# Kernel tuning notes

Measured on AMD Instinct MI355X. Metric: run time of the kernel, lower is better.

## Reference

```python
import jax, jax.numpy as jnp
import numpy as np

B, S, D, H = 4, 2048, 768, 12
HD = D // H
SCALE = HD ** -0.5


def setup_inputs() -> dict:
    key = jax.random.key(0)
    ks = jax.random.split(key, 9)
    std = D ** -0.5
    x = jax.random.normal(ks[0], (B, S, D), dtype=jnp.float32)
    Wq = jax.random.normal(ks[1], (D, D), dtype=jnp.float32) * std
    Wk = jax.random.normal(ks[2], (D, D), dtype=jnp.float32) * std
    Wv = jax.random.normal(ks[3], (D, D), dtype=jnp.float32) * std
    Wo = jax.random.normal(ks[4], (D, D), dtype=jnp.float32) * std
    bq = jax.random.normal(ks[5], (D,), dtype=jnp.float32) * 0.01
    bk = jax.random.normal(ks[6], (D,), dtype=jnp.float32) * 0.01
    bv = jax.random.normal(ks[7], (D,), dtype=jnp.float32) * 0.01
    bo = jax.random.normal(ks[8], (D,), dtype=jnp.float32) * 0.01
    return {"x": x, "Wq": Wq, "bq": bq, "Wk": Wk, "bk": bk,
            "Wv": Wv, "bv": bv, "Wo": Wo, "bo": bo}


def reference(x, Wq, bq, Wk, bk, Wv, bv, Wo, bo):
    b, s, _ = x.shape
    # projections (torch Linear: y = x @ W.T + b)
    q = (x @ Wq.T + bq).reshape(b, s, H, HD).transpose(0, 2, 1, 3)  # [B,H,S,HD]
    k = (x @ Wk.T + bk).reshape(b, s, H, HD).transpose(0, 2, 1, 3)
    v = (x @ Wv.T + bv).reshape(b, s, H, HD).transpose(0, 2, 1, 3)
    attn = jnp.einsum('bhqd,bhkd->bhqk', q, k) * SCALE
    attn = jax.nn.softmax(attn, axis=-1)  # dropout is identity in eval mode
    out = jnp.einsum('bhqk,bhkd->bhqd', attn, v)
    out = out.transpose(0, 2, 1, 3).reshape(b, s, D)
    return out @ Wo.T + bo
```

## Files before the change

kernel.cpp:

```cpp
#include <hip/hip_runtime.h>

#define LOG2E 1.4426950408889634f
#define QSCALE (0.125f * LOG2E)

typedef __attribute__((ext_vector_type(8))) __bf16 bf8_t;
typedef __attribute__((ext_vector_type(4))) float f4_t;

__device__ __forceinline__ unsigned short f2bf(float f) {
  unsigned int u = __float_as_uint(f);
  u += 0x7fff + ((u >> 16) & 1);
  return (unsigned short)(u >> 16);
}

__device__ __forceinline__ void async16(const void* g, void* l) {
  __builtin_amdgcn_global_load_lds(
      (const __attribute__((address_space(1))) void*)g,
      (__attribute__((address_space(3))) void*)l, 16, 0, 0);
}

__device__ __forceinline__ int swm(int r) {
  return ((r & 3) << 4) | ((r & 8) << 3);
}
__device__ __forceinline__ int swzoff(int row, int cb) {
  return (row << 7) + (cb ^ swm(row));
}

__global__ void cvt_multi(const float* __restrict__ x,
                          const float* __restrict__ w0, const float* __restrict__ w1,
                          const float* __restrict__ w2, const float* __restrict__ w3,
                          unsigned short* __restrict__ xb,
                          unsigned short* __restrict__ d0, unsigned short* __restrict__ d1,
                          unsigned short* __restrict__ d2, unsigned short* __restrict__ d3) {
  const int NX = 1572864;
  const int NW = 147456;
  const int total = NX + 4 * NW;
  int i = blockIdx.x * blockDim.x + threadIdx.x;
  int stride = gridDim.x * blockDim.x;
  for (; i < total; i += stride) {
    const float* s;
    unsigned short* d;
    int off;
    if (i < NX) {
      s = x; d = xb; off = i;
    } else {
      int j = i - NX;
      int wsel = j / NW;
      off = j - wsel * NW;
      s = (wsel == 0) ? w0 : (wsel == 1) ? w1 : (wsel == 2) ? w2 : w3;
      d = (wsel == 0) ? d0 : (wsel == 1) ? d1 : (wsel == 2) ? d2 : d3;
    }
    float4 v = ((const float4*)s)[off];
    ushort4 o;
    o.x = f2bf(v.x); o.y = f2bf(v.y); o.z = f2bf(v.z); o.w = f2bf(v.w);
    ((ushort4*)d)[off] = o;
  }
}

__device__ __forceinline__ void gemm_core(const unsigned short* __restrict__ A,
                                          const unsigned short* __restrict__ Bm,
                                          int i0, int j0,
                                          char* lsA, char* lsB,
                                          f4_t (&acc)[4][4]) {
  const int tid = threadIdx.x;
  const int l = tid & 63;
  const int wi = (tid >> 6) >> 1, wj = (tid >> 6) & 1;
  for (int k0 = 0; k0 < 768; k0 += 64) {
#pragma unroll
    for (int u = 0; u < 4; ++u) {
      int p = (u * 256 + tid) * 16;
      int r = p >> 7, cb = p & 127;
      int c = cb ^ swm(r);
      async16((const char*)A + ((size_t)(i0 + r) * 768 + k0) * 2 + c, lsA + p);
      async16((const char*)Bm + ((size_t)(j0 + r) * 768 + k0) * 2 + c, lsB + p);
    }
    __syncthreads();
#pragma unroll
    for (int ks = 0; ks < 2; ++ks) {
      bf8_t af[4], bfr[4];
#pragma unroll
      for (int mi = 0; mi < 4; ++mi)
        af[mi] = *(const bf8_t*)(lsA + swzoff(wi * 64 + mi * 16 + (l & 15),
                                              ks * 64 + ((l >> 4) << 4)));
#pragma unroll
      for (int nj = 0; nj < 4; ++nj)
        bfr[nj] = *(const bf8_t*)(lsB + swzoff(wj * 64 + nj * 16 + (l & 15),
                                               ks * 64 + ((l >> 4) << 4)));
      __builtin_amdgcn_s_setprio(1);
#pragma unroll
      for (int mi = 0; mi < 4; ++mi)
#pragma unroll
        for (int nj = 0; nj < 4; ++nj)
          acc[mi][nj] = __builtin_amdgcn_mfma_f32_16x16x32_bf16(
              af[mi], bfr[nj], acc[mi][nj], 0, 0, 0);
      __builtin_amdgcn_s_setprio(0);
    }
    __syncthreads();
  }
}

__global__ __launch_bounds__(256) void proj_qkv(
    const unsigned short* __restrict__ xb,
    const unsigned short* __restrict__ wq,
    const unsigned short* __restrict__ wk,
    const unsigned short* __restrict__ wv,
    const float* __restrict__ bq, const float* __restrict__ bk,
    const float* __restrict__ bv,
    unsigned short* __restrict__ qo, unsigned short* __restrict__ ko,
    unsigned short* __restrict__ vto) {
  __shared__ char lsA[16384], lsB[16384];
  const int bx = (blockIdx.x & 7) * 144 + (blockIdx.x >> 3);
  const int z = bx / 384, r = bx % 384;
  int it, jt;
  const unsigned short *A, *Bm;
  const float* bias;
  if (z == 0)      { A = wq; Bm = xb; bias = bq; it = r % 6;  jt = r / 6;  }
  else if (z == 1) { A = wk; Bm = xb; bias = bk; it = r % 6;  jt = r / 6;  }
  else             { A = xb; Bm = wv; bias = bv; it = r % 64; jt = r / 64; }
  const int i0 = it * 128, j0 = jt * 128;
  f4_t acc[4][4] = {};
  gemm_core(A, Bm, i0, j0, lsA, lsB, acc);

  const int tid = threadIdx.x, l = tid & 63;
  const int wi = (tid >> 6) >> 1, wj = (tid >> 6) & 1;
#pragma unroll
  for (int mi = 0; mi < 4; ++mi) {
#pragma unroll
    for (int nj = 0; nj < 4; ++nj) {
      int ib = i0 + wi * 64 + mi * 16 + ((l >> 4) << 2);
      int j  = j0 + wj * 64 + nj * 16 + (l & 15);
      f4_t v = acc[mi][nj];
      if (z < 2) {
        float4 bs = *(const float4*)(bias + ib);
        float sc = (z == 0) ? QSCALE : 1.0f;
        ushort4 o;
        o.x = f2bf((v[0] + bs.x) * sc);
        o.y = f2bf((v[1] + bs.y) * sc);
        o.z = f2bf((v[2] + bs.z) * sc);
        o.w = f2bf((v[3] + bs.w) * sc);
        int bb = j >> 11, s = j & 2047;
        int h = ib >> 6, d = ib & 63;
        unsigned short* dst = (z == 0) ? qo : ko;
        *(ushort4*)(dst + (((size_t)(bb * 12 + h) * 2048 + s) << 6) + d) = o;
      } else {
        float bvs = bias[j];
        ushort4 o;
        o.x = f2bf(v[0] + bvs); o.y = f2bf(v[1] + bvs);
        o.z = f2bf(v[2] + bvs); o.w = f2bf(v[3] + bvs);
        int bb = ib >> 11, s4 = ib & 2047;
        int h = j >> 6, d = j & 63;
        *(ushort4*)(vto + ((size_t)((bb * 12 + h) * 64 + d)) * 2048 + s4) = o;
      }
    }
  }
}

__global__ __launch_bounds__(256) void proj_o(
    const unsigned short* __restrict__ attnb, const unsigned short* __restrict__ wo,
    const float* __restrict__ bo, float* __restrict__ outp) {
  __shared__ char lsA[16384], lsB[16384];
  const int bx = (blockIdx.x & 7) * 48 + (blockIdx.x >> 3);
  const int it = bx % 6, jt = bx / 6;
  const int i0 = it * 128, j0 = jt * 128;
  f4_t acc[4][4] = {};
  gemm_core(wo, attnb, i0, j0, lsA, lsB, acc);
  const int tid = threadIdx.x, l = tid & 63;
  const int wi = (tid >> 6) >> 1, wj = (tid >> 6) & 1;
#pragma unroll
  for (int mi = 0; mi < 4; ++mi) {
#pragma unroll
    for (int nj = 0; nj < 4; ++nj) {
      int ib = i0 + wi * 64 + mi * 16 + ((l >> 4) << 2);
      int j  = j0 + wj * 64 + nj * 16 + (l & 15);
      float4 bs = *(const float4*)(bo + ib);
      float4 o;
      o.x = acc[mi][nj][0] + bs.x;
      o.y = acc[mi][nj][1] + bs.y;
      o.z = acc[mi][nj][2] + bs.z;
      o.w = acc[mi][nj][3] + bs.w;
      *(float4*)(outp + (size_t)j * 768 + ib) = o;
    }
  }
}

__global__ __launch_bounds__(512) void attn_kernel(
    const unsigned short* __restrict__ qg,
    const unsigned short* __restrict__ kg,
    const unsigned short* __restrict__ vtg,
    unsigned short* __restrict__ attnb) {
  __shared__ char ls[65536];
  const int tid = threadIdx.x, l = tid & 63, w = tid >> 6;
  const int qw = w & 3, hf = w >> 2;
  const int swz = (blockIdx.x & 7) * 96 + (blockIdx.x >> 3);
  const int q0 = (swz & 15) * 128;
  const int bh = swz >> 4;
  const size_t qkbase = (size_t)bh * 2048 * 64;
  const size_t vtbase = (size_t)bh * 64 * 2048;

#pragma unroll
  for (int u = 0; u < 2; ++u) {
    int p = (u * 512 + tid) * 16;
    int r = p >> 7, cb = p & 127;
    int c = cb ^ swm(r);
    async16((const char*)qg + (qkbase + (size_t)(q0 + r) * 64) * 2 + c, ls + p);
  }
  __syncthreads();
  bf8_t qf[2][2];
#pragma unroll
  for (int qt = 0; qt < 2; ++qt)
#pragma unroll
    for (int ks = 0; ks < 2; ++ks)
      qf[qt][ks] = *(const bf8_t*)(ls + swzoff(qw * 32 + qt * 16 + (l & 15),
                                               ks * 64 + ((l >> 4) << 4)));
  __syncthreads();

  const int p16 = tid * 16;
  const int sr = p16 >> 7;
  const int sc = (p16 & 127) ^ swm(sr);
  async16((const char*)kg + (qkbase + (size_t)sr * 64) * 2 + sc, ls + p16);
  async16((const char*)vtg + (vtbase + (size_t)sr * 2048) * 2 + sc,
          ls + 8192 + p16);
  async16((const char*)kg + (qkbase + (size_t)(64 + sr) * 64) * 2 + sc,
          ls + 16384 + p16);
  async16((const char*)vtg + (vtbase + (size_t)sr * 2048 + 64) * 2 + sc,
          ls + 16384 + 8192 + p16);
  const char* gKa = (const char*)kg + (qkbase + (size_t)(128 + sr) * 64) * 2 + sc;
  const char* gVa = (const char*)vtg + (vtbase + (size_t)sr * 2048 + 128) * 2 + sc;
  const char* gKb = gKa + 8192;
  const char* gVb = gVa + 128;
  __syncthreads();

  int koff[4][2];
#pragma unroll
  for (int kt = 0; kt < 4; ++kt) {
    int i = l & 15;
    int row = ((kt >> 1) << 5) + ((kt & 1) << 2) + ((i >> 2) << 3) + (i & 3);
#pragma unroll
    for (int ks = 0; ks < 2; ++ks)
      koff[kt][ks] = swzoff(row, ks * 64 + ((l >> 4) << 4));
  }
  int voff[4][2];
#pragma unroll
  for (int dt = 0; dt < 4; ++dt)
#pragma unroll
    for (int ks = 0; ks < 2; ++ks)
      voff[dt][ks] = swzoff(dt * 16 + (l & 15), ks * 64 + ((l >> 4) << 4));

  bf8_t onesf;
#pragma unroll
  for (int e = 0; e < 8; ++e) onesf[e] = (__bf16)1.0f;

  f4_t acc[4][2] = {};
  f4_t accs[2] = {};

  for (int i = 0; i < 16; ++i) {
    if (i < 15) {
      char* dst = ls + (((i + 1) & 1) * 2) * 16384;
      async16(gKa, dst + p16);
      async16(gVa, dst + 8192 + p16);
      async16(gKb, dst + 16384 + p16);
      async16(gVb, dst + 16384 + 8192 + p16);
      gKa += 16384; gKb += 16384;
      gVa += 256;   gVb += 256;
    }
    const char* bK = ls + ((i & 1) * 2 + hf) * 16384;
    const char* bV = bK + 8192;

    f4_t sacc[4][2] = {};
    __builtin_amdgcn_s_setprio(1);
#pragma unroll
    for (int kt = 0; kt < 4; ++kt)
#pragma unroll
      for (int ks = 0; ks < 2; ++ks) {
        bf8_t a = *(const bf8_t*)(bK + koff[kt][ks]);
#pragma unroll
        for (int qt = 0; qt < 2; ++qt)
          sacc[kt][qt] = __builtin_amdgcn_mfma_f32_16x16x32_bf16(
              a, qf[qt][ks], sacc[kt][qt], 0, 0, 0);
      }
    __builtin_amdgcn_s_setprio(0);

    bf8_t pf[2][2];
#pragma unroll
    for (int qt = 0; qt < 2; ++qt)
#pragma unroll
      for (int ks = 0; ks < 2; ++ks)
#pragma unroll
        for (int e = 0; e < 8; ++e)
          pf[ks][qt][e] =
              (__bf16)__builtin_amdgcn_exp2f(sacc[2 * ks + (e >> 2)][qt][e & 3]);

    __builtin_amdgcn_s_setprio(1);
#pragma unroll
    for (int dt = 0; dt < 4; ++dt) {
      bf8_t av0 = *(const bf8_t*)(bV + voff[dt][0]);
      bf8_t av1 = *(const bf8_t*)(bV + voff[dt][1]);
#pragma unroll
      for (int qt = 0; qt < 2; ++qt) {
        acc[dt][qt] = __builtin_amdgcn_mfma_f32_16x16x32_bf16(av0, pf[0][qt],
                                                              acc[dt][qt], 0, 0, 0);
        acc[dt][qt] = __builtin_amdgcn_mfma_f32_16x16x32_bf16(av1, pf[1][qt],
                                                              acc[dt][qt], 0, 0, 0);
      }
    }
#pragma unroll
    for (int qt = 0; qt < 2; ++qt) {
      accs[qt] = __builtin_amdgcn_mfma_f32_16x16x32_bf16(onesf, pf[0][qt],
                                                         accs[qt], 0, 0, 0);
      accs[qt] = __builtin_amdgcn_mfma_f32_16x16x32_bf16(onesf, pf[1][qt],
                                                         accs[qt], 0, 0, 0);
    }
    __builtin_amdgcn_s_setprio(0);
    __syncthreads();
  }

  char* reg_ = ls + qw * 8704;
  if (hf) {
#pragma unroll
    for (int dt = 0; dt < 4; ++dt)
#pragma unroll
      for (int qt = 0; qt < 2; ++qt)
        *(f4_t*)(reg_ + (((dt * 2 + qt) * 64) + l) * 16) = acc[dt][qt];
    *(float2*)(reg_ + 8192 + l * 8) = float2{accs[0][0], accs[1][0]};
  }
  __syncthreads();
  if (!hf) {
    const int bb = bh / 12, h = bh % 12;
    float2 os = *(const float2*)(reg_ + 8192 + l * 8);
    float inv0 = 1.0f / (accs[0][0] + os.x);
    float inv1 = 1.0f / (accs[1][0] + os.y);
#pragma unroll
    for (int qt = 0; qt < 2; ++qt) {
      float inv = qt ? inv1 : inv0;
      int s = q0 + qw * 32 + qt * 16 + (l & 15);
#pragma unroll
      for (int dt = 0; dt < 4; ++dt) {
        f4_t other = *(const f4_t*)(reg_ + (((dt * 2 + qt) * 64) + l) * 16);
        int dg = h * 64 + dt * 16 + ((l >> 4) << 2);
        ushort4 o;
        o.x = f2bf((acc[dt][qt][0] + other[0]) * inv);
        o.y = f2bf((acc[dt][qt][1] + other[1]) * inv);
        o.z = f2bf((acc[dt][qt][2] + other[2]) * inv);
        o.w = f2bf((acc[dt][qt][3] + other[3]) * inv);
        *(ushort4*)(attnb + ((size_t)(bb * 2048 + s)) * 768 + dg) = o;
      }
    }
  }
}

extern "C" void kernel_launch(void* const* d_in, const int* in_sizes, int n_in,
                              void* d_out, int out_size, void* d_ws, size_t ws_size,
                              hipStream_t stream) {
  const float* x  = (const float*)d_in[0];
  const float* Wq = (const float*)d_in[1];
  const float* bq = (const float*)d_in[2];
  const float* Wk = (const float*)d_in[3];
  const float* bk = (const float*)d_in[4];
  const float* Wv = (const float*)d_in[5];
  const float* bv = (const float*)d_in[6];
  const float* Wo = (const float*)d_in[7];
  const float* bo = (const float*)d_in[8];

  const size_t XB_ELEMS = (size_t)8192 * 768;
  const size_t W_ELEMS  = (size_t)768 * 768;
  unsigned short* xb  = (unsigned short*)d_ws;
  unsigned short* wqb = xb  + XB_ELEMS;
  unsigned short* wkb = wqb + W_ELEMS;
  unsigned short* wvb = wkb + W_ELEMS;
  unsigned short* wob = wvb + W_ELEMS;
  unsigned short* qb  = wob + W_ELEMS;
  unsigned short* kb  = qb  + XB_ELEMS;
  unsigned short* vtb = kb  + XB_ELEMS;
  unsigned short* attnb = xb;

  cvt_multi<<<2048, 256, 0, stream>>>(x, Wq, Wk, Wv, Wo,
                                      xb, wqb, wkb, wvb, wob);
  proj_qkv<<<1152, 256, 0, stream>>>(xb, wqb, wkb, wvb, bq, bk, bv, qb, kb, vtb);
  attn_kernel<<<768, 512, 0, stream>>>(qb, kb, vtb, attnb);
  proj_o<<<384, 256, 0, stream>>>(attnb, wob, bo, (float*)d_out);
}
```

Baseline: 145.2 us.

## Double-buffer GEMM LDS staging and stage projection epilogue through shared memory

The shared GEMM core now uses two 32KB LDS buffers, prefetching the next K-slice asynchronously while MFMAs run on the current one, instead of load-then-sync each step. The QKV projection remaps blocks so each token tile handles Q, K and V slices together, improving reuse of x tiles in cache. Its epilogue writes results into swizzled LDS and then emits coalesced 16-byte row stores for Q/K and the transposed V. This doubles LDS per block to 64KB, which may reduce occupancy.

```diff
diff --git a/kernel.cpp b/kernel.cpp
--- a/kernel.cpp
+++ b/kernel.cpp
@@ -58,22 +58,28 @@
 
 __device__ __forceinline__ void gemm_core(const unsigned short* __restrict__ A,
                                           const unsigned short* __restrict__ Bm,
-                                          int i0, int j0,
-                                          char* lsA, char* lsB,
+                                          int i0, int j0, char* ls,
                                           f4_t (&acc)[4][4]) {
   const int tid = threadIdx.x;
   const int l = tid & 63;
   const int wi = (tid >> 6) >> 1, wj = (tid >> 6) & 1;
-  for (int k0 = 0; k0 < 768; k0 += 64) {
+  auto stage = [&](int buf, int k0) {
+    char* dA = ls + buf * 32768;
+    char* dB = dA + 16384;
 #pragma unroll
     for (int u = 0; u < 4; ++u) {
       int p = (u * 256 + tid) * 16;
-      int r = p >> 7, cb = p & 127;
-      int c = cb ^ swm(r);
-      async16((const char*)A + ((size_t)(i0 + r) * 768 + k0) * 2 + c, lsA + p);
-      async16((const char*)Bm + ((size_t)(j0 + r) * 768 + k0) * 2 + c, lsB + p);
-    }
-    __syncthreads();
+      int r = p >> 7, c = (p & 127) ^ swm(r);
+      async16((const char*)A + ((size_t)(i0 + r) * 768 + k0) * 2 + c, dA + p);
+      async16((const char*)Bm + ((size_t)(j0 + r) * 768 + k0) * 2 + c, dB + p);
+    }
+  };
+  stage(0, 0);
+  __syncthreads();
+  for (int kk = 0; kk < 12; ++kk) {
+    if (kk < 11) stage((kk + 1) & 1, (kk + 1) * 64);
+    const char* lsA = ls + (kk & 1) * 32768;
+    const char* lsB = lsA + 16384;
 #pragma unroll
     for (int ks = 0; ks < 2; ++ks) {
       bf8_t af[4], bfr[4];
@@ -107,18 +113,20 @@
     const float* __restrict__ bv,
     unsigned short* __restrict__ qo, unsigned short* __restrict__ ko,
     unsigned short* __restrict__ vto) {
-  __shared__ char lsA[16384], lsB[16384];
+  __shared__ char ls[65536];
   const int bx = (blockIdx.x & 7) * 144 + (blockIdx.x >> 3);
-  const int z = bx / 384, r = bx % 384;
-  int it, jt;
+  const int mt = bx / 18, nt = bx % 18;
+  const int sec = nt / 6, nn = nt % 6;
+  const int nbase = nn * 128;
+  const int mbase = mt * 128;
   const unsigned short *A, *Bm;
-  const float* bias;
-  if (z == 0)      { A = wq; Bm = xb; bias = bq; it = r % 6;  jt = r / 6;  }
-  else if (z == 1) { A = wk; Bm = xb; bias = bk; it = r % 6;  jt = r / 6;  }
-  else             { A = xb; Bm = wv; bias = bv; it = r % 64; jt = r / 64; }
-  const int i0 = it * 128, j0 = jt * 128;
+  if (sec == 0)      { A = wq; Bm = xb; }
+  else if (sec == 1) { A = wk; Bm = xb; }
+  else               { A = xb; Bm = wv; }
+  const int gi0 = (sec == 2) ? mbase : nbase;
+  const int gj0 = (sec == 2) ? nbase : mbase;
   f4_t acc[4][4] = {};
-  gemm_core(A, Bm, i0, j0, lsA, lsB, acc);
+  gemm_core(A, Bm, gi0, gj0, ls, acc);
 
   const int tid = threadIdx.x, l = tid & 63;
   const int wi = (tid >> 6) >> 1, wj = (tid >> 6) & 1;
@@ -126,30 +134,50 @@
   for (int mi = 0; mi < 4; ++mi) {
 #pragma unroll
     for (int nj = 0; nj < 4; ++nj) {
-      int ib = i0 + wi * 64 + mi * 16 + ((l >> 4) << 2);
-      int j  = j0 + wj * 64 + nj * 16 + (l & 15);
+      int ib = wi * 64 + mi * 16 + ((l >> 4) << 2);
+      int j  = wj * 64 + nj * 16 + (l & 15);
       f4_t v = acc[mi][nj];
-      if (z < 2) {
-        float4 bs = *(const float4*)(bias + ib);
-        float sc = (z == 0) ? QSCALE : 1.0f;
-        ushort4 o;
+      ushort4 o;
+      if (sec < 2) {
+        const float* bias = sec ? bk : bq;
+        float sc = sec ? 1.0f : QSCALE;
+        float4 bs = *(const float4*)(bias + nbase + ib);
         o.x = f2bf((v[0] + bs.x) * sc);
         o.y = f2bf((v[1] + bs.y) * sc);
         o.z = f2bf((v[2] + bs.z) * sc);
         o.w = f2bf((v[3] + bs.w) * sc);
-        int bb = j >> 11, s = j & 2047;
-        int h = ib >> 6, d = ib & 63;
-        unsigned short* dst = (z == 0) ? qo : ko;
-        *(ushort4*)(dst + (((size_t)(bb * 12 + h) * 2048 + s) << 6) + d) = o;
       } else {
-        float bvs = bias[j];
-        ushort4 o;
+        float bvs = bv[nbase + j];
         o.x = f2bf(v[0] + bvs); o.y = f2bf(v[1] + bvs);
         o.z = f2bf(v[2] + bvs); o.w = f2bf(v[3] + bvs);
-        int bb = ib >> 11, s4 = ib & 2047;
-        int h = j >> 6, d = j & 63;
-        *(ushort4*)(vto + ((size_t)((bb * 12 + h) * 64 + d)) * 2048 + s4) = o;
       }
+      int chunk = (ib >> 3) ^ (j & 15);
+      *(ushort4*)(ls + j * 256 + chunk * 16 + ((ib & 7) << 1)) = o;
+    }
+  }
+  __syncthreads();
+  const int row = tid >> 1, half = tid & 1;
+  if (sec < 2) {
+    int sg = mbase + row;
+    int b = sg >> 11, s = sg & 2047;
+    int h = nn * 2 + half;
+    unsigned short* dst = (sec ? ko : qo) + (((size_t)(b * 12 + h) * 2048 + s) << 6);
+#pragma unroll
+    for (int c = 0; c < 8; ++c) {
+      int cb = half * 8 + c;
+      uint4 v = *(const uint4*)(ls + row * 256 + ((cb ^ (row & 15)) << 4));
+      ((uint4*)dst)[c] = v;
+    }
+  } else {
+    int h = nn * 2 + (row >> 6), dh = row & 63;
+    int b = mt >> 4;
+    int scol = (mt & 15) * 128 + half * 64;
+    unsigned short* dst = vto + ((size_t)((b * 12 + h) * 64 + dh)) * 2048 + scol;
+#pragma unroll
+    for (int c = 0; c < 8; ++c) {
+      int cb = half * 8 + c;
+      uint4 v = *(const uint4*)(ls + row * 256 + ((cb ^ (row & 15)) << 4));
+      ((uint4*)dst)[c] = v;
     }
   }
 }
@@ -157,12 +185,12 @@
 __global__ __launch_bounds__(256) void proj_o(
     const unsigned short* __restrict__ attnb, const unsigned short* __restrict__ wo,
     const float* __restrict__ bo, float* __restrict__ outp) {
-  __shared__ char lsA[16384], lsB[16384];
+  __shared__ char ls[65536];
   const int bx = (blockIdx.x & 7) * 48 + (blockIdx.x >> 3);
   const int it = bx % 6, jt = bx / 6;
   const int i0 = it * 128, j0 = jt * 128;
   f4_t acc[4][4] = {};
-  gemm_core(wo, attnb, i0, j0, lsA, lsB, acc);
+  gemm_core(wo, attnb, i0, j0, ls, acc);
   const int tid = threadIdx.x, l = tid & 63;
   const int wi = (tid >> 6) >> 1, wj = (tid >> 6) & 1;
 #pragma unroll
```

Result: faster. 138.1 us (-4.9%).
